# Kernel optimization log

Measured on AMD Instinct MI355X. Metric: run time of the kernel, lower is better.

The kernel has to match this reference:

```python
import jax, jax.numpy as jnp
import numpy as np


def _centers(n):
    # make_coord_3d: cell-center coordinates in (-1, 1)
    r = 1.0 / n
    return -1.0 + r + 2.0 * r * jnp.arange(n, dtype=jnp.float32)


def setup_inputs() -> dict:
    key = jax.random.key(0)
    ks = jax.random.split(key, 16)
    B, C, Tin, Hin, Win = 1, 64, 6, 40, 40
    Gc = 27 + 8 * C  # 539 channels into conv00_3d
    s = lambda k, shp: jax.random.normal(k, shp, dtype=jnp.float32) * 0.05
    return {
        "feat": jax.random.normal(ks[0], (B, C, Tin, Hin, Win), dtype=jnp.float32),
        # conv00_3d = depthwise(1x1x1, groups=Gc) + pointwise(Gc->256)
        "dw1_w": s(ks[1], (Gc,)), "dw1_b": s(ks[2], (Gc,)),
        "pw1_w": s(ks[3], (256, Gc)), "pw1_b": s(ks[4], (256,)),
        "fc1_w": s(ks[5], (256, 256)), "fc1_b": s(ks[6], (256,)),
        "fc2_w": s(ks[7], (3, 256)), "fc2_b": s(ks[8], (3,)),
        # short_cut = depthwise(1x1x1, groups=C) + pointwise(C->3)
        "sc_dw_w": s(ks[9], (C,)), "sc_dw_b": s(ks[10], (C,)),
        "sc_pw_w": s(ks[11], (3, C)), "sc_pw_b": s(ks[12], (3,)),
        "T_out": 12, "H_out": 80, "W_out": 80,
    }


def _pw(x, w, b):
    # 1x1x1 Conv3d
    return jnp.einsum('bcthw,oc->bothw', x, w) + b[None, :, None, None, None]


def _forward(feat, dw1_w, dw1_b, pw1_w, pw1_b, fc1_w, fc1_b, fc2_w, fc2_b,
             sc_dw_w, sc_dw_b, sc_pw_w, sc_pw_b, T_out, H_out, W_out):
    B, C, Tin, Hin, Win = feat.shape
    ct, ch, cw = _centers(T_out), _centers(H_out), _centers(W_out)  # target centers
    lt, lh, lw = _centers(Tin), _centers(Hin), _centers(Win)        # low-res centers
    rt, rx, ry = 1.0 / Tin, 1.0 / Hin, 1.0 / Win                    # 2/N/2 radii
    eps = 1e-6

    def near(c, n):
        # grid_sample nearest, align_corners=False; coords pre-clamped as in torch code
        cc = jnp.clip(c, -1.0 + 1e-6, 1.0 - 1e-6)
        return jnp.clip(jnp.round(((cc + 1.0) * n - 1.0) / 2.0), 0, n - 1).astype(jnp.int32)

    rel_coords, feat_s, areas = [], [], []
    for vt in (-1.0, 1.0):
        for vx in (-1.0, 1.0):
            for vy in (-1.0, 1.0):
                it = near(ct + vt * rt + eps, Tin)   # [T'] (separable per-dim)
                ih = near(ch + vx * rx + eps, Hin)   # [H']
                iw = near(cw + vy * ry + eps, Win)   # [W']
                f = feat[:, :, it[:, None, None], ih[None, :, None], iw[None, None, :]]
                dct = (ct - lt[it]) * Tin
                dch = (ch - lh[ih]) * Hin
                dcw = (cw - lw[iw]) * Win
                rel = jnp.stack([
                    jnp.broadcast_to(dct[:, None, None], (T_out, H_out, W_out)),
                    jnp.broadcast_to(dch[None, :, None], (T_out, H_out, W_out)),
                    jnp.broadcast_to(dcw[None, None, :], (T_out, H_out, W_out)),
                ], axis=0)
                rel = jnp.broadcast_to(rel[None], (B, 3, T_out, H_out, W_out))
                area = (jnp.abs(dct)[:, None, None] * jnp.abs(dch)[None, :, None]
                        * jnp.abs(dcw)[None, None, :]) + 1e-9
                rel_coords.append(rel)
                feat_s.append(f)
                areas.append(area)

    tot = sum(areas)
    areas_sw = areas[::-1]  # pairwise swaps 0<->7, 1<->6, 2<->5, 3<->4
    feat_s = [f * (a / tot)[None, None] for f, a in zip(feat_s, areas_sw)]

    # rel_cell: (2/size * scale) * in_size == 2.0 on every axis
    rel_cell = jnp.full((B, 3, T_out, H_out, W_out), 2.0, dtype=feat.dtype)

    grid = jnp.concatenate([*rel_coords, *feat_s, rel_cell], axis=1)  # [B,27+8C,T',H',W']

    x = _pw(grid * dw1_w[None, :, None, None, None] + dw1_b[None, :, None, None, None],
            pw1_w, pw1_b)
    ret = _pw(jax.nn.gelu(_pw(x, fc1_w, fc1_b), approximate=False), fc2_w, fc2_b)

    # short cut: depthwise-separable 1x1x1 conv, then trilinear grid_sample (border pad)
    sc = _pw(feat * sc_dw_w[None, :, None, None, None] + sc_dw_b[None, :, None, None, None],
             sc_pw_w, sc_pw_b)

    def lin_idx(c, n):
        x = jnp.clip(((c + 1.0) * n - 1.0) / 2.0, 0.0, n - 1.0)  # border padding: clip coord
        x0 = jnp.floor(x)
        frac = x - x0
        i0 = x0.astype(jnp.int32)
        i1 = jnp.minimum(i0 + 1, n - 1)
        return i0, i1, frac

    t0, t1, ft = lin_idx(ct, Tin)
    h0, h1, fh = lin_idx(ch, Hin)
    w0, w1, fw = lin_idx(cw, Win)
    g = sc[:, :, t0] * (1 - ft)[None, None, :, None, None] + sc[:, :, t1] * ft[None, None, :, None, None]
    g = g[:, :, :, h0] * (1 - fh)[None, None, None, :, None] + g[:, :, :, h1] * fh[None, None, None, :, None]
    g = g[:, :, :, :, w0] * (1 - fw) + g[:, :, :, :, w1] * fw
    return ret + g


def reference(feat, dw1_w, dw1_b, pw1_w, pw1_b, fc1_w, fc1_b, fc2_w, fc2_b,
              sc_dw_w, sc_dw_b, sc_pw_w, sc_pw_b, T_out, H_out, W_out):
    return _forward(feat, dw1_w, dw1_b, pw1_w, pw1_b, fc1_w, fc1_b, fc2_w, fc2_b,
                    sc_dw_w, sc_dw_b, sc_pw_w, sc_pw_b, T_out, H_out, W_out)
```

## Files before the change

kernel.cpp:

```cpp
#include <hip/hip_runtime.h>
#include <hip/hip_bf16.h>

using bf16 = __hip_bfloat16;
typedef __attribute__((ext_vector_type(8))) short short8x;
typedef __attribute__((ext_vector_type(4))) short short4x;
typedef __attribute__((ext_vector_type(4))) unsigned short ushort4x;
typedef __attribute__((ext_vector_type(4))) float f32x4;

__device__ __forceinline__ float b2f(bf16 x) { return __bfloat162float(x); }
__device__ __forceinline__ bf16  f2b(float x) { return __float2bfloat16(x); }
__device__ __forceinline__ short bbits(float x) { bf16 b = f2b(x); short s; __builtin_memcpy(&s, &b, 2); return s; }
__device__ __forceinline__ float bu2f(unsigned short s) {
    unsigned v = ((unsigned)s) << 16; float f; __builtin_memcpy(&f, &v, 4); return f;
}
__device__ __forceinline__ float ldin(const void* p, int i, int f32) {
    return f32 ? ((const float*)p)[i] : b2f(((const bf16*)p)[i]);
}

#define TI 6
#define HI 40
#define WI 40
#define TO 12
#define HO 80
#define WO 80
#define NIN (TI*HI*WI)
#define NOUT (TO*HO*WO)

#define F_B1    0
#define F_ACO   (F_B1 + 256)
#define F_SCW   (F_ACO + 6*256)
#define F_SCB   (F_SCW + 3*64)
#define F_SC    (F_SCB + 4)
#define F_DT    (F_SC + 3*NIN)
#define F_DH    (F_DT + 2*TO)
#define F_DW    (F_DH + 2*HO)
#define F_FT    (F_DW + 2*WO)
#define F_FH    (F_FT + TO)
#define F_FW    (F_FH + HO)
#define F_FC1B  (F_FW + WO)
#define F_FC2W  (F_FC1B + 256)
#define F_FC2B  (F_FC2W + 768)
#define F_END   (F_FC2B + 4)
#define I_IT    0
#define I_IH    (I_IT + 2*TO)
#define I_IW    (I_IH + 2*HO)
#define I_LT0   (I_IW + 2*WO)
#define I_LT1   (I_LT0 + TO)
#define I_LH0   (I_LT1 + TO)
#define I_LH1   (I_LH0 + HO)
#define I_LW0   (I_LH1 + HO)
#define I_LW1   (I_LW0 + WO)
#define I_FLAG  (I_LW1 + WO)
#define I_END   (I_FLAG + 1)

#define MPOS 32
#define ZPAD 264
#define FT_S 72

__device__ __forceinline__ void axis_tables(int i, int n_out, int n_in,
                                            float* dvals, int* ivals,
                                            int* l0, int* l1, float* fr) {
    const float r_out = 1.0f / (float)n_out;
    const float r_in  = 1.0f / (float)n_in;
    const float c = -1.0f + r_out + 2.0f * r_out * (float)i;
    #pragma unroll
    for (int v = 0; v < 2; ++v) {
        const float vv = v ? 1.0f : -1.0f;
        float cc = c + vv * r_in + 1e-6f;
        cc = fminf(fmaxf(cc, -1.0f + 1e-6f), 1.0f - 1e-6f);
        float fx = rintf(((cc + 1.0f) * (float)n_in - 1.0f) * 0.5f);
        fx = fminf(fmaxf(fx, 0.0f), (float)(n_in - 1));
        const int idx = (int)fx;
        const float l = -1.0f + r_in + 2.0f * r_in * (float)idx;
        dvals[v * n_out + i] = (c - l) * (float)n_in;
        ivals[v * n_out + i] = idx;
    }
    float x = fminf(fmaxf(((c + 1.0f) * (float)n_in - 1.0f) * 0.5f, 0.0f), (float)(n_in - 1));
    const float x0 = floorf(x);
    fr[i] = x - x0;
    const int i0 = (int)x0;
    l0[i] = i0;
    l1[i] = min(i0 + 1, n_in - 1);
}

__global__ __launch_bounds__(256)
void k_setup(const void* __restrict__ feat,
             const void* __restrict__ dw1_w, const void* __restrict__ dw1_b,
             const void* __restrict__ pw1_w, const void* __restrict__ pw1_b,
             const void* __restrict__ fc1_w, const void* __restrict__ fc1_b,
             const void* __restrict__ fc2_w, const void* __restrict__ fc2_b,
             const void* __restrict__ sc_dw_w, const void* __restrict__ sc_dw_b,
             const void* __restrict__ sc_pw_w, const void* __restrict__ sc_pw_b,
             bf16* __restrict__ fc1P, bf16* __restrict__ W1fP,
             float* __restrict__ F, int* __restrict__ I) {
    const int tid = threadIdx.x;
    const int b = blockIdx.x;
    __shared__ int sflag;
    if (tid < 64) {
        const unsigned short* u = (const unsigned short*)feat;
        const unsigned e = (u[2 * tid] >> 7) & 0xFFu;
        const unsigned long long m = __ballot(e >= 0x68u && e <= 0x8Eu);
        if (tid == 0) sflag = (__popcll(m) < 32) ? 1 : 0;
    }
    __syncthreads();
    const int f32 = sflag;

    if (b >= 288) {
        const int g = (b - 288) * 256 + tid;
        const int k = g >> 11, kc = (g >> 10) & 1, nt = (g >> 6) & 15, wl = g & 63;
        const int n = nt * 16 + (wl & 15);
        const int k0 = kc * 32 + (wl >> 4) * 8;
        bf16 v[8];
        #pragma unroll
        for (int jj = 0; jj < 8; ++jj) {
            const int ch = 24 + k * 64 + k0 + jj;
            v[jj] = f2b(ldin(pw1_w, n * 539 + ch, f32) * ldin(dw1_w, ch, f32));
        }
        *(short8x*)&W1fP[(size_t)g * 8] = *(short8x*)v;
        return;
    }
    if (b >= 256) {
        const int g = (b - 256) * 256 + tid;
        const int kc = g >> 10, nt = (g >> 6) & 15, wl = g & 63;
        const int n = nt * 16 + (wl & 15);
        const int k0 = kc * 32 + (wl >> 4) * 8;
        bf16 v[8];
        #pragma unroll
        for (int jj = 0; jj < 8; ++jj) v[jj] = f2b(ldin(fc1_w, n * 256 + k0 + jj, f32));
        *(short8x*)&fc1P[(size_t)g * 8] = *(short8x*)v;
        return;
    }

    __shared__ float row[539];
    __shared__ float red[256];
    const int o = b;

    for (int ch = tid; ch < 539; ch += 256) row[ch] = ldin(pw1_w, o * 539 + ch, f32);
    __syncthreads();

    float s = 0.f;
    for (int ch = tid; ch < 539; ch += 256) s += row[ch] * ldin(dw1_b, ch, f32);
    red[tid] = s;
    __syncthreads();
    for (int st = 128; st > 0; st >>= 1) {
        if (tid < st) red[tid] += red[tid + st];
        __syncthreads();
    }

    if (tid == 0) {
        float bacc = ldin(pw1_b, o, f32) + red[0];
        #pragma unroll
        for (int ch = 536; ch < 539; ++ch)
            bacc += 2.0f * row[ch] * ldin(dw1_w, ch, f32);
        F[F_B1 + o] = bacc;

        float A[6] = {0.f, 0.f, 0.f, 0.f, 0.f, 0.f};
        #pragma unroll
        for (int k = 0; k < 8; ++k) {
            A[(k >> 2)]           += row[3*k + 0] * ldin(dw1_w, 3*k + 0, f32);
            A[2 + ((k >> 1) & 1)] += row[3*k + 1] * ldin(dw1_w, 3*k + 1, f32);
            A[4 + (k & 1)]        += row[3*k + 2] * ldin(dw1_w, 3*k + 2, f32);
        }
        #pragma unroll
        for (int i = 0; i < 6; ++i) F[F_ACO + i * 256 + o] = A[i];
    }

    if (b == 0) {
        if (tid == 0) I[I_FLAG] = f32;
        F[F_FC1B + tid] = ldin(fc1_b, tid, f32);
        for (int r = tid; r < 768; r += 256) F[F_FC2W + r] = ldin(fc2_w, r, f32);
        if (tid < 3) F[F_FC2B + tid] = ldin(fc2_b, tid, f32);
        if (tid < 3) {
            const int j = tid;
            float sb = ldin(sc_pw_b, j, f32);
            for (int c = 0; c < 64; ++c) {
                const float pw = ldin(sc_pw_w, j * 64 + c, f32);
                F[F_SCW + j * 64 + c] = pw * ldin(sc_dw_w, c, f32);
                sb += pw * ldin(sc_dw_b, c, f32);
            }
            F[F_SCB + j] = sb;
        }
        if (tid < TO) axis_tables(tid, TO, TI, F + F_DT, I + I_IT, I + I_LT0, I + I_LT1, F + F_FT);
        if (tid < HO) axis_tables(tid, HO, HI, F + F_DH, I + I_IH, I + I_LH0, I + I_LH1, F + F_FH);
        if (tid < WO) axis_tables(tid, WO, WI, F + F_DW, I + I_IW, I + I_LW0, I + I_LW1, F + F_FW);
    }
}

__global__ __launch_bounds__(256)
void k_corner(const void* __restrict__ feat, float* __restrict__ F,
              const int* __restrict__ I, const bf16* __restrict__ W1fP,
              bf16* __restrict__ P) {
    const int tid = threadIdx.x;
    const int pt = blockIdx.x, k = blockIdx.y;
    const int pos0 = pt * 32;
    const int f32 = I[I_FLAG];

    __shared__ __align__(16) short ft[32 * FT_S];
    __shared__ __align__(16) short zt[32 * ZPAD];

    {
        const int p = tid & 31, c0 = tid >> 5;
        #pragma unroll
        for (int cc = 0; cc < 8; ++cc) {
            const int c = c0 * 8 + cc;
            ft[p * FT_S + c] = bbits(ldin(feat, c * NIN + pos0 + p, f32));
        }
    }
    __syncthreads();

    const int wl = tid & 63, w = tid >> 6;
    const int col = wl & 15, quad = wl >> 4;
    f32x4 acc[2][4] = { { {0,0,0,0},{0,0,0,0},{0,0,0,0},{0,0,0,0} },
                        { {0,0,0,0},{0,0,0,0},{0,0,0,0},{0,0,0,0} } };
    const short8x* bp = (const short8x*)W1fP;
    #pragma unroll
    for (int kc = 0; kc < 2; ++kc) {
        const short8x a0 = *(const short8x*)&ft[col * FT_S + kc * 32 + quad * 8];
        const short8x a1 = *(const short8x*)&ft[(col + 16) * FT_S + kc * 32 + quad * 8];
        #pragma unroll
        for (int nt = 0; nt < 4; ++nt) {
            const short8x bb = bp[((k * 2 + kc) * 16 + (w * 4 + nt)) * 64 + wl];
            acc[0][nt] = __builtin_amdgcn_mfma_f32_16x16x32_bf16(a0, bb, acc[0][nt], 0, 0, 0);
            acc[1][nt] = __builtin_amdgcn_mfma_f32_16x16x32_bf16(a1, bb, acc[1][nt], 0, 0, 0);
        }
    }

    if (k == 0 && tid < 96) {
        const int j = tid >> 5, p = tid & 31;
        float s = F[F_SCB + j];
        for (int c = 0; c < 64; ++c)
            s += bu2f((unsigned short)ft[p * FT_S + c]) * F[F_SCW + j * 64 + c];
        F[F_SC + j * NIN + pos0 + p] = s;
    }

    #pragma unroll
    for (int mt = 0; mt < 2; ++mt)
        #pragma unroll
        for (int nt = 0; nt < 4; ++nt) {
            const int n = w * 64 + nt * 16 + col;
            #pragma unroll
            for (int r = 0; r < 4; ++r)
                zt[(mt * 16 + quad * 4 + r) * ZPAD + n] = bbits(acc[mt][nt][r]);
        }
    __syncthreads();

    #pragma unroll
    for (int q = 0; q < 4; ++q) {
        const int i = q * 256 + tid;
        const int p = i >> 5, c8 = i & 31;
        const short8x v = *(const short8x*)&zt[p * ZPAD + c8 * 8];
        *(short8x*)(P + ((size_t)(k * NIN + pos0 + p)) * 256 + c8 * 8) = v;
    }
}

__global__ __launch_bounds__(256, 4)
void k_main(const bf16* __restrict__ P, const bf16* __restrict__ fc1P,
            const float* __restrict__ F, const int* __restrict__ I,
            void* __restrict__ outv) {
    const int tid = threadIdx.x;
    const int pos0 = blockIdx.x * MPOS;
    const int f32 = I[I_FLAG];

    __shared__ __align__(16) short zsh[MPOS * ZPAD];
    __shared__ float redc[MPOS * 4 * 3];
    __shared__ int   sh_ipos[MPOS][8];
    __shared__ float sh_wk[MPOS][8];
    __shared__ float sh_dv[MPOS][6];
    __shared__ float sh_g[3][MPOS];

    if (tid < MPOS) {
        const int p = tid;
        const int pos = pos0 + p;
        const int t = pos / (HO * WO);
        const int rem = pos - t * (HO * WO);
        const int h = rem / WO;
        const int w = rem - h * WO;
        const int   iTa[2] = { I[I_IT + t], I[I_IT + TO + t] };
        const float dTv[2] = { F[F_DT + t], F[F_DT + TO + t] };
        const int   iHa[2] = { I[I_IH + h], I[I_IH + HO + h] };
        const float dHv[2] = { F[F_DH + h], F[F_DH + HO + h] };
        const int   iWa[2] = { I[I_IW + w], I[I_IW + WO + w] };
        const float dWv[2] = { F[F_DW + w], F[F_DW + WO + w] };
        sh_dv[p][0] = dTv[0]; sh_dv[p][1] = dTv[1];
        sh_dv[p][2] = dHv[0]; sh_dv[p][3] = dHv[1];
        sh_dv[p][4] = dWv[0]; sh_dv[p][5] = dWv[1];
        const float aT[2] = { fabsf(dTv[0]), fabsf(dTv[1]) };
        const float aH[2] = { fabsf(dHv[0]), fabsf(dHv[1]) };
        const float aW[2] = { fabsf(dWv[0]), fabsf(dWv[1]) };
        const float tot = (aT[0] + aT[1]) * (aH[0] + aH[1]) * (aW[0] + aW[1]) + 8e-9f;
        #pragma unroll
        for (int k = 0; k < 8; ++k) {
            const int at = k >> 2, ah = (k >> 1) & 1, aw = k & 1;
            sh_wk[p][k] = (aT[1 - at] * aH[1 - ah] * aW[1 - aw] + 1e-9f) / tot;
            sh_ipos[p][k] = iTa[at] * (HI * WI) + iHa[ah] * WI + iWa[aw];
        }
        const int a0 = I[I_LT0 + t], a1 = I[I_LT1 + t];
        const int bh0 = I[I_LH0 + h], bh1 = I[I_LH1 + h];
        const int c0 = I[I_LW0 + w], c1 = I[I_LW1 + w];
        const float fT = F[F_FT + t], fH = F[F_FH + h], fW = F[F_FW + w];
        #pragma unroll
        for (int jj = 0; jj < 3; ++jj) {
            const float* Sj = F + F_SC + jj * NIN;
            const int i0 = a0 * (HI * WI), i1 = a1 * (HI * WI);
            const float v000 = Sj[i0 + bh0 * WI + c0], v001 = Sj[i0 + bh0 * WI + c1];
            const float v010 = Sj[i0 + bh1 * WI + c0], v011 = Sj[i0 + bh1 * WI + c1];
            const float v100 = Sj[i1 + bh0 * WI + c0], v101 = Sj[i1 + bh0 * WI + c1];
            const float v110 = Sj[i1 + bh1 * WI + c0], v111 = Sj[i1 + bh1 * WI + c1];
            const float u00 = v000 * (1.f - fT) + v100 * fT;
            const float u01 = v001 * (1.f - fT) + v101 * fT;
            const float u10 = v010 * (1.f - fT) + v110 * fT;
            const float u11 = v011 * (1.f - fT) + v111 * fT;
            const float q0 = u00 * (1.f - fH) + u10 * fH;
            const float q1 = u01 * (1.f - fH) + u11 * fH;
            sh_g[jj][p] = q0 * (1.f - fW) + q1 * fW;
        }
    }
    __syncthreads();

    {
        const int og = tid & 63, pg = tid >> 6;
        const int o4 = og * 4;
        const float4 bz = *(const float4*)&F[F_B1 + o4];
        float4 Ac[6];
        #pragma unroll
        for (int i = 0; i < 6; ++i) Ac[i] = *(const float4*)&F[F_ACO + i * 256 + o4];
        for (int pp = 0; pp < 8; ++pp) {
            const int p = pg * 8 + pp;
            float a0 = bz.x, a1 = bz.y, a2 = bz.z, a3 = bz.w;
            #pragma unroll
            for (int i = 0; i < 6; ++i) {
                const float dv = sh_dv[p][i];
                a0 += Ac[i].x * dv; a1 += Ac[i].y * dv;
                a2 += Ac[i].z * dv; a3 += Ac[i].w * dv;
            }
            #pragma unroll
            for (int k = 0; k < 8; ++k) {
                const float wk = sh_wk[p][k];
                const ushort4x u = *(const ushort4x*)(P + ((size_t)(k * NIN + sh_ipos[p][k]) * 256 + o4));
                a0 += wk * bu2f(u.x); a1 += wk * bu2f(u.y);
                a2 += wk * bu2f(u.z); a3 += wk * bu2f(u.w);
            }
            short4x zz = { bbits(a0), bbits(a1), bbits(a2), bbits(a3) };
            *(short4x*)&zsh[p * ZPAD + o4] = zz;
        }
    }
    __syncthreads();

    {
        const int wl = tid & 63, w = tid >> 6;
        const int col = wl & 15, quad = wl >> 4;
        f32x4 acc0[4] = { {0,0,0,0}, {0,0,0,0}, {0,0,0,0}, {0,0,0,0} };
        f32x4 acc1[4] = { {0,0,0,0}, {0,0,0,0}, {0,0,0,0}, {0,0,0,0} };
        const short8x* bp = (const short8x*)fc1P;
        #pragma unroll
        for (int kc = 0; kc < 8; ++kc) {
            const short8x a0 = *(const short8x*)&zsh[col * ZPAD + kc * 32 + quad * 8];
            const short8x a1 = *(const short8x*)&zsh[(col + 16) * ZPAD + kc * 32 + quad * 8];
            #pragma unroll
            for (int nt = 0; nt < 4; ++nt) {
                const short8x b = bp[(kc * 16 + w * 4 + nt) * 64 + wl];
                acc0[nt] = __builtin_amdgcn_mfma_f32_16x16x32_bf16(a0, b, acc0[nt], 0, 0, 0);
                acc1[nt] = __builtin_amdgcn_mfma_f32_16x16x32_bf16(a1, b, acc1[nt], 0, 0, 0);
            }
        }
        float part[2][3][4];
        #pragma unroll
        for (int mt = 0; mt < 2; ++mt)
            #pragma unroll
            for (int jj = 0; jj < 3; ++jj)
                #pragma unroll
                for (int r = 0; r < 4; ++r) part[mt][jj][r] = 0.f;
        #pragma unroll
        for (int nt = 0; nt < 4; ++nt) {
            const int j = w * 64 + nt * 16 + col;
            const float fb = F[F_FC1B + j];
            const float w0 = F[F_FC2W + j];
            const float w1 = F[F_FC2W + 256 + j];
            const float w2 = F[F_FC2W + 512 + j];
            #pragma unroll
            for (int r = 0; r < 4; ++r) {
                float x = acc0[nt][r] + fb;
                float hh = 0.5f * x * (1.0f + erff(x * 0.70710678118654752f));
                part[0][0][r] += w0 * hh; part[0][1][r] += w1 * hh; part[0][2][r] += w2 * hh;
                x = acc1[nt][r] + fb;
                hh = 0.5f * x * (1.0f + erff(x * 0.70710678118654752f));
                part[1][0][r] += w0 * hh; part[1][1][r] += w1 * hh; part[1][2][r] += w2 * hh;
            }
        }
        #pragma unroll
        for (int m = 1; m <= 8; m <<= 1)
            #pragma unroll
            for (int mt = 0; mt < 2; ++mt)
                #pragma unroll
                for (int jj = 0; jj < 3; ++jj)
                    #pragma unroll
                    for (int r = 0; r < 4; ++r)
                        part[mt][jj][r] += __shfl_xor(part[mt][jj][r], m, 64);
        if (col == 0) {
            #pragma unroll
            for (int mt = 0; mt < 2; ++mt)
                #pragma unroll
                for (int jj = 0; jj < 3; ++jj)
                    #pragma unroll
                    for (int r = 0; r < 4; ++r) {
                        const int p = mt * 16 + quad * 4 + r;
                        redc[(p * 4 + w) * 3 + jj] = part[mt][jj][r];
                    }
        }
    }
    __syncthreads();

    if (tid < 96) {
        const int p = tid / 3, jj = tid - 3 * p;
        float a = F[F_FC2B + jj] + sh_g[jj][p];
        #pragma unroll
        for (int w = 0; w < 4; ++w) a += redc[(p * 4 + w) * 3 + jj];
        const int oidx = jj * NOUT + pos0 + p;
        if (f32) ((float*)outv)[oidx] = a;
        else     ((bf16*)outv)[oidx] = f2b(a);
    }
}

extern "C" void kernel_launch(void* const* d_in, const int* in_sizes, int n_in,
                              void* d_out, int out_size, void* d_ws, size_t ws_size,
                              hipStream_t stream) {
    const void* feat    = d_in[0];
    const void* dw1_w   = d_in[1];
    const void* dw1_b   = d_in[2];
    const void* pw1_w   = d_in[3];
    const void* pw1_b   = d_in[4];
    const void* fc1_w   = d_in[5];
    const void* fc1_b   = d_in[6];
    const void* fc2_w   = d_in[7];
    const void* fc2_b   = d_in[8];
    const void* sc_dw_w = d_in[9];
    const void* sc_dw_b = d_in[10];
    const void* sc_pw_w = d_in[11];
    const void* sc_pw_b = d_in[12];

    const size_t P_BYTES    = (size_t)8 * NIN * 256 * 2;
    const size_t FC1P_BYTES = (size_t)256 * 256 * 2;
    const size_t W1FP_BYTES = (size_t)8 * 64 * 256 * 2;
    bf16*  P    = (bf16*)d_ws;
    bf16*  fc1P = (bf16*)((char*)d_ws + P_BYTES);
    bf16*  W1fP = (bf16*)((char*)d_ws + P_BYTES + FC1P_BYTES);
    float* F    = (float*)((char*)d_ws + P_BYTES + FC1P_BYTES + W1FP_BYTES);
    int*   I    = (int*)(F + F_END);

    k_setup<<<352, 256, 0, stream>>>(feat, dw1_w, dw1_b, pw1_w, pw1_b, fc1_w, fc1_b,
                                     fc2_w, fc2_b, sc_dw_w, sc_dw_b, sc_pw_w, sc_pw_b,
                                     fc1P, W1fP, F, I);
    k_corner<<<dim3(NIN / 32, 8), 256, 0, stream>>>(feat, F, I, W1fP, P);
    k_main<<<NOUT / MPOS, 256, 0, stream>>>(P, fc1P, F, I, (void*)d_out);
}
```

Baseline: 171.9 us.

## Fold fc1 into the pointwise conv weights so corner tables produce fc1 pre-activations

Uses linearity to precompute fc1·pw1 composite weights (and folded biases/coord coefficients) so the per-corner table Q already holds fc1 outputs. The main kernel then only gathers and blends Q, applies a polynomial erf-based GELU and the 3-wide fc2 projection, removing the per-output 256x256 MFMA GEMM and its LDS staging. The composite-weight setup now does a 256-length dot product per element, corner blocks handle two corners each, and a fast approximate erf replaces erff, which adds some numeric error.

After: 269.6 us. 1.57x slower.

```diff
diff --git a/kernel.cpp b/kernel.cpp
--- a/kernel.cpp
+++ b/kernel.cpp
@@ -15,6 +15,22 @@
 }
 __device__ __forceinline__ float ldin(const void* p, int i, int f32) {
     return f32 ? ((const float*)p)[i] : b2f(((const bf16*)p)[i]);
+}
+
+__device__ __forceinline__ float gelu_f(float x) {
+    const float u = x * 0.70710678118654752f;
+    const float z = fabsf(u);
+    const float t = __builtin_amdgcn_rcpf(fmaf(0.3275911f, z, 1.0f));
+    float pl = fmaf(1.061405429f, t, -1.453152027f);
+    pl = fmaf(pl, t, 1.421413741f);
+    pl = fmaf(pl, t, -0.284496736f);
+    pl = fmaf(pl, t, 0.254829592f);
+    pl *= t;
+    const float e = __builtin_amdgcn_exp2f((z * z) * -1.4426950408889634f);
+    float er = fmaf(-pl, e, 1.0f);
+    er = __builtin_copysignf(er, u);
+    const float g = 0.5f * x;
+    return fmaf(g, er, g);
 }
 
 #define TI 6
@@ -37,10 +53,11 @@
 #define F_FT    (F_DW + 2*WO)
 #define F_FH    (F_FT + TO)
 #define F_FW    (F_FH + HO)
-#define F_FC1B  (F_FW + WO)
-#define F_FC2W  (F_FC1B + 256)
+#define F_FC2W  (F_FW + WO)
 #define F_FC2B  (F_FC2W + 768)
-#define F_END   (F_FC2B + 4)
+#define F_B2    (F_FC2B + 4)
+#define F_A2    (F_B2 + 256)
+#define F_END   (F_A2 + 6*256)
 #define I_IT    0
 #define I_IH    (I_IT + 2*TO)
 #define I_IW    (I_IH + 2*HO)
@@ -91,8 +108,7 @@
              const void* __restrict__ fc2_w, const void* __restrict__ fc2_b,
              const void* __restrict__ sc_dw_w, const void* __restrict__ sc_dw_b,
              const void* __restrict__ sc_pw_w, const void* __restrict__ sc_pw_b,
-             bf16* __restrict__ fc1P, bf16* __restrict__ W1fP,
-             float* __restrict__ F, int* __restrict__ I) {
+             bf16* __restrict__ WqP, float* __restrict__ F, int* __restrict__ I) {
     const int tid = threadIdx.x;
     const int b = blockIdx.x;
     __shared__ int sflag;
@@ -105,29 +121,23 @@
     __syncthreads();
     const int f32 = sflag;
 
-    if (b >= 288) {
-        const int g = (b - 288) * 256 + tid;
+    if (b >= 256) {
+        const int g = (b - 256) * 256 + tid;
         const int k = g >> 11, kc = (g >> 10) & 1, nt = (g >> 6) & 15, wl = g & 63;
         const int n = nt * 16 + (wl & 15);
-        const int k0 = kc * 32 + (wl >> 4) * 8;
+        const int ch0 = 24 + k * 64 + kc * 32 + (wl >> 4) * 8;
+        float acc[8] = {0.f,0.f,0.f,0.f,0.f,0.f,0.f,0.f};
+        for (int o = 0; o < 256; ++o) {
+            const float f = ldin(fc1_w, n * 256 + o, f32);
+            #pragma unroll
+            for (int jj = 0; jj < 8; ++jj)
+                acc[jj] = fmaf(f, ldin(pw1_w, o * 539 + ch0 + jj, f32), acc[jj]);
+        }
         bf16 v[8];
         #pragma unroll
-        for (int jj = 0; jj < 8; ++jj) {
-            const int ch = 24 + k * 64 + k0 + jj;
-            v[jj] = f2b(ldin(pw1_w, n * 539 + ch, f32) * ldin(dw1_w, ch, f32));
-        }
-        *(short8x*)&W1fP[(size_t)g * 8] = *(short8x*)v;
-        return;
-    }
-    if (b >= 256) {
-        const int g = (b - 256) * 256 + tid;
-        const int kc = g >> 10, nt = (g >> 6) & 15, wl = g & 63;
-        const int n = nt * 16 + (wl & 15);
-        const int k0 = kc * 32 + (wl >> 4) * 8;
-        bf16 v[8];
-        #pragma unroll
-        for (int jj = 0; jj < 8; ++jj) v[jj] = f2b(ldin(fc1_w, n * 256 + k0 + jj, f32));
-        *(short8x*)&fc1P[(size_t)g * 8] = *(short8x*)v;
+        for (int jj = 0; jj < 8; ++jj)
+            v[jj] = f2b(acc[jj] * ldin(dw1_w, ch0 + jj, f32));
+        *(short8x*)&WqP[(size_t)g * 8] = *(short8x*)v;
         return;
     }
 
@@ -167,7 +177,6 @@
 
     if (b == 0) {
         if (tid == 0) I[I_FLAG] = f32;
-        F[F_FC1B + tid] = ldin(fc1_b, tid, f32);
         for (int r = tid; r < 768; r += 256) F[F_FC2W + r] = ldin(fc2_w, r, f32);
         if (tid < 3) F[F_FC2B + tid] = ldin(fc2_b, tid, f32);
         if (tid < 3) {
@@ -187,14 +196,32 @@
 }
 
 __global__ __launch_bounds__(256)
-void k_corner(const void* __restrict__ feat, float* __restrict__ F,
-              const int* __restrict__ I, const bf16* __restrict__ W1fP,
-              bf16* __restrict__ P) {
+void k_corner(const void* __restrict__ feat,
+              const void* __restrict__ fc1_w, const void* __restrict__ fc1_b,
+              float* __restrict__ F, const int* __restrict__ I,
+              const bf16* __restrict__ WqP, bf16* __restrict__ Q) {
     const int tid = threadIdx.x;
-    const int pt = blockIdx.x, k = blockIdx.y;
+    const int pt = blockIdx.x, y = blockIdx.y;
+    const int f32 = I[I_FLAG];
+
+    if (pt == 300) {
+        if (y != 0) return;
+        const int j = tid;
+        float accB = ldin(fc1_b, j, f32);
+        float accA[6] = {0.f,0.f,0.f,0.f,0.f,0.f};
+        for (int o = 0; o < 256; ++o) {
+            const float f = ldin(fc1_w, j * 256 + o, f32);
+            accB = fmaf(f, F[F_B1 + o], accB);
+            #pragma unroll
+            for (int i = 0; i < 6; ++i) accA[i] = fmaf(f, F[F_ACO + i * 256 + o], accA[i]);
+        }
+        F[F_B2 + j] = accB;
+        #pragma unroll
+        for (int i = 0; i < 6; ++i) F[F_A2 + i * 256 + j] = accA[i];
+        return;
+    }
+
     const int pos0 = pt * 32;
-    const int f32 = I[I_FLAG];
-
     __shared__ __align__(16) short ft[32 * FT_S];
     __shared__ __align__(16) short zt[32 * ZPAD];
 
@@ -210,63 +237,77 @@
 
     const int wl = tid & 63, w = tid >> 6;
     const int col = wl & 15, quad = wl >> 4;
-    f32x4 acc[2][4] = { { {0,0,0,0},{0,0,0,0},{0,0,0,0},{0,0,0,0} },
-                        { {0,0,0,0},{0,0,0,0},{0,0,0,0},{0,0,0,0} } };
-    const short8x* bp = (const short8x*)W1fP;
+    const short8x* bp = (const short8x*)WqP;
+
     #pragma unroll
-    for (int kc = 0; kc < 2; ++kc) {
-        const short8x a0 = *(const short8x*)&ft[col * FT_S + kc * 32 + quad * 8];
-        const short8x a1 = *(const short8x*)&ft[(col + 16) * FT_S + kc * 32 + quad * 8];
-        #pragma unroll
-        for (int nt = 0; nt < 4; ++nt) {
-            const short8x bb = bp[((k * 2 + kc) * 16 + (w * 4 + nt)) * 64 + wl];
-            acc[0][nt] = __builtin_amdgcn_mfma_f32_16x16x32_bf16(a0, bb, acc[0][nt], 0, 0, 0);
-            acc[1][nt] = __builtin_amdgcn_mfma_f32_16x16x32_bf16(a1, bb, acc[1][nt], 0, 0, 0);
-        }
-    }
-
-    if (k == 0 && tid < 96) {
-        const int j = tid >> 5, p = tid & 31;
-        float s = F[F_SCB + j];
-        for (int c = 0; c < 64; ++c)
-            s += bu2f((unsigned short)ft[p * FT_S + c]) * F[F_SCW + j * 64 + c];
-        F[F_SC + j * NIN + pos0 + p] = s;
-    }
-
-    #pragma unroll
-    for (int mt = 0; mt < 2; ++mt)
-        #pragma unroll
-        for (int nt = 0; nt < 4; ++nt) {
-            const int n = w * 64 + nt * 16 + col;
+    for (int c2 = 0; c2 < 2; ++c2) {
+        const int k = y * 2 + c2;
+        f32x4 acc[2][4] = { { {0,0,0,0},{0,0,0,0},{0,0,0,0},{0,0,0,0} },
+                            { {0,0,0,0},{0,0,0,0},{0,0,0,0},{0,0,0,0} } };
+        #pragma unroll
+        for (int kc = 0; kc < 2; ++kc) {
+            const short8x a0 = *(const short8x*)&ft[col * FT_S + kc * 32 + quad * 8];
+            const short8x a1 = *(const short8x*)&ft[(col + 16) * FT_S + kc * 32 + quad * 8];
             #pragma unroll
-            for (int r = 0; r < 4; ++r)
-                zt[(mt * 16 + quad * 4 + r) * ZPAD + n] = bbits(acc[mt][nt][r]);
-        }
-    __syncthreads();
-
-    #pragma unroll
-    for (int q = 0; q < 4; ++q) {
-        const int i = q * 256 + tid;
-        const int p = i >> 5, c8 = i & 31;
-        const short8x v = *(const short8x*)&zt[p * ZPAD + c8 * 8];
-        *(short8x*)(P + ((size_t)(k * NIN + pos0 + p)) * 256 + c8 * 8) = v;
+            for (int nt = 0; nt < 4; ++nt) {
+                const short8x bb = bp[((k * 2 + kc) * 16 + (w * 4 + nt)) * 64 + wl];
+                acc[0][nt] = __builtin_amdgcn_mfma_f32_16x16x32_bf16(a0, bb, acc[0][nt], 0, 0, 0);
+                acc[1][nt] = __builtin_amdgcn_mfma_f32_16x16x32_bf16(a1, bb, acc[1][nt], 0, 0, 0);
+            }
+        }
+
+        if (c2 == 0 && y == 0 && tid < 96) {
+            const int j = tid >> 5, p = tid & 31;
+            float s = F[F_SCB + j];
+            for (int c = 0; c < 64; ++c)
+                s += bu2f((unsigned short)ft[p * FT_S + c]) * F[F_SCW + j * 64 + c];
+            F[F_SC + j * NIN + pos0 + p] = s;
+        }
+
+        #pragma unroll
+        for (int mt = 0; mt < 2; ++mt)
+            #pragma unroll
+            for (int nt = 0; nt < 4; ++nt) {
+                const int n = w * 64 + nt * 16 + col;
+                #pragma unroll
+                for (int r = 0; r < 4; ++r)
+                    zt[(mt * 16 + quad * 4 + r) * ZPAD + n] = bbits(acc[mt][nt][r]);
+            }
+        __syncthreads();
+
+        #pragma unroll
+        for (int q = 0; q < 4; ++q) {
+            const int i = q * 256 + tid;
+            const int p = i >> 5, c8 = i & 31;
+            const short8x v = *(const short8x*)&zt[p * ZPAD + c8 * 8];
+            *(short8x*)(Q + ((size_t)(k * NIN + pos0 + p)) * 256 + c8 * 8) = v;
+        }
+        __syncthreads();
     }
 }
 
 __global__ __launch_bounds__(256, 4)
-void k_main(const bf16* __restrict__ P, const bf16* __restrict__ fc1P,
-            const float* __restrict__ F, const int* __restrict__ I,
-            void* __restrict__ outv) {
+void k_main(const bf16* __restrict__ Q, const float* __restrict__ F,
+            const int* __restrict__ I, void* __restrict__ outv) {
     const int tid = threadIdx.x;
     const int pos0 = blockIdx.x * MPOS;
     const int f32 = I[I_FLAG];
 
-    __shared__ __align__(16) short zsh[MPOS * ZPAD];
-    __shared__ float redc[MPOS * 4 * 3];
     __shared__ int   sh_ipos[MPOS][8];
     __shared__ float sh_wk[MPOS][8];
     __shared__ float sh_dv[MPOS][6];
     __shared__ float sh_g[3][MPOS];
+    __shared__ float redc[4][4][8][3];
+
+    const int og = tid & 63, pg = tid >> 6;
+    const int j4 = og * 4;
+    const float4 b2v = *(const float4*)&F[F_B2 + j4];
+    float4 A2v[6];
+    #pragma unroll
+    for (int i = 0; i < 6; ++i) A2v[i] = *(const float4*)&F[F_A2 + i * 256 + j4];
+    const float4 fw0 = *(const float4*)&F[F_FC2W + j4];
+    const float4 fw1 = *(const float4*)&F[F_FC2W + 256 + j4];
+    const float4 fw2 = *(const float4*)&F[F_FC2W + 512 + j4];
 
     if (tid < MPOS) {
         const int p = tid;
@@ -317,95 +358,38 @@
     }
     __syncthreads();
 
-    {
-        const int og = tid & 63, pg = tid >> 6;
-        const int o4 = og * 4;
-        const float4 bz = *(const float4*)&F[F_B1 + o4];
-        float4 Ac[6];
-        #pragma unroll
-        for (int i = 0; i < 6; ++i) Ac[i] = *(const float4*)&F[F_ACO + i * 256 + o4];
-        for (int pp = 0; pp < 8; ++pp) {
-            const int p = pg * 8 + pp;
-            float a0 = bz.x, a1 = bz.y, a2 = bz.z, a3 = bz.w;
-            #pragma unroll
-            for (int i = 0; i < 6; ++i) {
-                const float dv = sh_dv[p][i];
-                a0 += Ac[i].x * dv; a1 += Ac[i].y * dv;
-                a2 += Ac[i].z * dv; a3 += Ac[i].w * dv;
-            }
-            #pragma unroll
-            for (int k = 0; k < 8; ++k) {
-                const float wk = sh_wk[p][k];
-                const ushort4x u = *(const ushort4x*)(P + ((size_t)(k * NIN + sh_ipos[p][k]) * 256 + o4));
-                a0 += wk * bu2f(u.x); a1 += wk * bu2f(u.y);
-                a2 += wk * bu2f(u.z); a3 += wk * bu2f(u.w);
-            }
-            short4x zz = { bbits(a0), bbits(a1), bbits(a2), bbits(a3) };
-            *(short4x*)&zsh[p * ZPAD + o4] = zz;
-        }
-    }
-    __syncthreads();
-
-    {
-        const int wl = tid & 63, w = tid >> 6;
-        const int col = wl & 15, quad = wl >> 4;
-        f32x4 acc0[4] = { {0,0,0,0}, {0,0,0,0}, {0,0,0,0}, {0,0,0,0} };
-        f32x4 acc1[4] = { {0,0,0,0}, {0,0,0,0}, {0,0,0,0}, {0,0,0,0} };
-        const short8x* bp = (const short8x*)fc1P;
-        #pragma unroll
-        for (int kc = 0; kc < 8; ++kc) {
-            const short8x a0 = *(const short8x*)&zsh[col * ZPAD + kc * 32 + quad * 8];
-            const short8x a1 = *(const short8x*)&zsh[(col + 16) * ZPAD + kc * 32 + quad * 8];
-            #pragma unroll
-            for (int nt = 0; nt < 4; ++nt) {
-                const short8x b = bp[(kc * 16 + w * 4 + nt) * 64 + wl];
-                acc0[nt] = __builtin_amdgcn_mfma_f32_16x16x32_bf16(a0, b, acc0[nt], 0, 0, 0);
-                acc1[nt] = __builtin_amdgcn_mfma_f32_16x16x32_bf16(a1, b, acc1[nt], 0, 0, 0);
-            }
-        }
-        float part[2][3][4];
-        #pragma unroll
-        for (int mt = 0; mt < 2; ++mt)
-            #pragma unroll
-            for (int jj = 0; jj < 3; ++jj)
-                #pragma unroll
-                for (int r = 0; r < 4; ++r) part[mt][jj][r] = 0.f;
-        #pragma unroll
-        for (int nt = 0; nt < 4; ++nt) {
-            const int j = w * 64 + nt * 16 + col;
-            const float fb = F[F_FC1B + j];
-            const float w0 = F[F_FC2W + j];
-            const float w1 = F[F_FC2W + 256 + j];
-            const float w2 = F[F_FC2W + 512 + j];
-            #pragma unroll
-            for (int r = 0; r < 4; ++r) {
-                float x = acc0[nt][r] + fb;
-                float hh = 0.5f * x * (1.0f + erff(x * 0.70710678118654752f));
-                part[0][0][r] += w0 * hh; part[0][1][r] += w1 * hh; part[0][2][r] += w2 * hh;
-                x = acc1[nt][r] + fb;
-                hh = 0.5f * x * (1.0f + erff(x * 0.70710678118654752f));
-                part[1][0][r] += w0 * hh; part[1][1][r] += w1 * hh; part[1][2][r] += w2 * hh;
-            }
-        }
-        #pragma unroll
-        for (int m = 1; m <= 8; m <<= 1)
-            #pragma unroll
-            for (int mt = 0; mt < 2; ++mt)
-                #pragma unroll
-                for (int jj = 0; jj < 3; ++jj)
-                    #pragma unroll
-                    for (int r = 0; r < 4; ++r)
-                        part[mt][jj][r] += __shfl_xor(part[mt][jj][r], m, 64);
-        if (col == 0) {
-            #pragma unroll
-            for (int mt = 0; mt < 2; ++mt)
-                #pragma unroll
-                for (int jj = 0; jj < 3; ++jj)
-                    #pragma unroll
-                    for (int r = 0; r < 4; ++r) {
-                        const int p = mt * 16 + quad * 4 + r;
-                        redc[(p * 4 + w) * 3 + jj] = part[mt][jj][r];
-                    }
+    #pragma unroll
+    for (int pp = 0; pp < 8; ++pp) {
+        const int p = pg * 8 + pp;
+        float a0 = b2v.x, a1 = b2v.y, a2 = b2v.z, a3 = b2v.w;
+        #pragma unroll
+        for (int i = 0; i < 6; ++i) {
+            const float dv = sh_dv[p][i];
+            a0 = fmaf(A2v[i].x, dv, a0); a1 = fmaf(A2v[i].y, dv, a1);
+            a2 = fmaf(A2v[i].z, dv, a2); a3 = fmaf(A2v[i].w, dv, a3);
+        }
+        #pragma unroll
+        for (int k = 0; k < 8; ++k) {
+            const float wk = sh_wk[p][k];
+            const ushort4x u = *(const ushort4x*)(Q + ((size_t)(k * NIN + sh_ipos[p][k])) * 256 + j4);
+            a0 = fmaf(wk, bu2f(u.x), a0); a1 = fmaf(wk, bu2f(u.y), a1);
+            a2 = fmaf(wk, bu2f(u.z), a2); a3 = fmaf(wk, bu2f(u.w), a3);
+        }
+        const float h0 = gelu_f(a0), h1 = gelu_f(a1), h2 = gelu_f(a2), h3 = gelu_f(a3);
+        float pj0 = h0 * fw0.x; pj0 = fmaf(h1, fw0.y, pj0); pj0 = fmaf(h2, fw0.z, pj0); pj0 = fmaf(h3, fw0.w, pj0);
+        float pj1 = h0 * fw1.x; pj1 = fmaf(h1, fw1.y, pj1); pj1 = fmaf(h2, fw1.z, pj1); pj1 = fmaf(h3, fw1.w, pj1);
+        float pj2 = h0 * fw2.x; pj2 = fmaf(h1, fw2.y, pj2); pj2 = fmaf(h2, fw2.z, pj2); pj2 = fmaf(h3, fw2.w, pj2);
+        #pragma unroll
+        for (int m = 1; m <= 8; m <<= 1) {
+            pj0 += __shfl_xor(pj0, m, 64);
+            pj1 += __shfl_xor(pj1, m, 64);
+            pj2 += __shfl_xor(pj2, m, 64);
+        }
+        if ((og & 15) == 0) {
+            const int grp = og >> 4;
+            redc[pg][grp][pp][0] = pj0;
+            redc[pg][grp][pp][1] = pj1;
+            redc[pg][grp][pp][2] = pj2;
         }
     }
     __syncthreads();
@@ -414,7 +398,7 @@
         const int p = tid / 3, jj = tid - 3 * p;
         float a = F[F_FC2B + jj] + sh_g[jj][p];
         #pragma unroll
-        for (int w = 0; w < 4; ++w) a += redc[(p * 4 + w) * 3 + jj];
+        for (int g4 = 0; g4 < 4; ++g4) a += redc[p >> 3][g4][p & 7][jj];
         const int oidx = jj * NOUT + pos0 + p;
         if (f32) ((float*)outv)[oidx] = a;
         else     ((bf16*)outv)[oidx] = f2b(a);
@@ -438,18 +422,16 @@
     const void* sc_pw_w = d_in[11];
     const void* sc_pw_b = d_in[12];
 
-    const size_t P_BYTES    = (size_t)8 * NIN * 256 * 2;
-    const size_t FC1P_BYTES = (size_t)256 * 256 * 2;
-    const size_t W1FP_BYTES = (size_t)8 * 64 * 256 * 2;
-    bf16*  P    = (bf16*)d_ws;
-    bf16*  fc1P = (bf16*)((char*)d_ws + P_BYTES);
-    bf16*  W1fP = (bf16*)((char*)d_ws + P_BYTES + FC1P_BYTES);
-    float* F    = (float*)((char*)d_ws + P_BYTES + FC1P_BYTES + W1FP_BYTES);
+    const size_t Q_BYTES   = (size_t)8 * NIN * 256 * 2;
+    const size_t WQP_BYTES = (size_t)16384 * 8 * 2;
+    bf16*  Q    = (bf16*)d_ws;
+    bf16*  WqP  = (bf16*)((char*)d_ws + Q_BYTES);
+    float* F    = (float*)((char*)d_ws + Q_BYTES + WQP_BYTES);
     int*   I    = (int*)(F + F_END);
 
-    k_setup<<<352, 256, 0, stream>>>(feat, dw1_w, dw1_b, pw1_w, pw1_b, fc1_w, fc1_b,
+    k_setup<<<320, 256, 0, stream>>>(feat, dw1_w, dw1_b, pw1_w, pw1_b, fc1_w, fc1_b,
                                      fc2_w, fc2_b, sc_dw_w, sc_dw_b, sc_pw_w, sc_pw_b,
-                                     fc1P, W1fP, F, I);
-    k_corner<<<dim3(NIN / 32, 8), 256, 0, stream>>>(feat, F, I, W1fP, P);
-    k_main<<<NOUT / MPOS, 256, 0, stream>>>(P, fc1P, F, I, (void*)d_out);
-}
+                                     WqP, F, I);
+    k_corner<<<dim3(301, 4), 256, 0, stream>>>(feat, fc1_w, fc1_b, F, I, WqP, Q);
+    k_main<<<NOUT / MPOS, 256, 0, stream>>>(Q, F, I, (void*)d_out);
+}
```
